# Kernel optimization log

Measured on AMD Instinct MI355X. Metric: run time of the kernel, lower is better.

The kernel has to match this reference:

```python
import jax, jax.numpy as jnp
import numpy as np

B, L, E, H = 2, 2048, 1024, 16
D = E // H  # head_dim = 64


def setup_inputs() -> dict:
    key = jax.random.key(0)
    ks = jax.random.split(key, 9)
    s = 1.0 / np.sqrt(E)
    return {
        "query": jax.random.normal(ks[0], (B, L, E), jnp.float32),
        "key": jax.random.normal(ks[1], (B, L, E), jnp.float32),
        "value": jax.random.normal(ks[2], (B, L, E), jnp.float32),
        # torch Linear weights are [out_features, in_features]
        "Wq": jax.random.uniform(ks[3], (E, E), jnp.float32, -s, s),
        "bq": jnp.zeros((E,), jnp.float32),
        "Wk": jax.random.uniform(ks[4], (E, E), jnp.float32, -s, s),  # k_proj, no bias (add_bias_kv=False)
        "Wv": jax.random.uniform(ks[5], (E, E), jnp.float32, -s, s),  # v_proj, no bias
        "Wo": jax.random.uniform(ks[6], (E, E), jnp.float32, -s, s),
        "bo": jnp.zeros((E,), jnp.float32),
    }


def reference(query, key, value, Wq, bq, Wk, Wv, Wo, bo):
    # Projections (torch Linear: y = x @ W.T + b)
    q = query @ Wq.T + bq          # [B, L, E]
    k = key @ Wk.T                 # [B, L, E]
    v = value @ Wv.T               # [B, L, E]
    # Split heads
    q = q.reshape(B, L, H, D)
    k = k.reshape(B, L, H, D)
    v = v.reshape(B, L, H, D)
    # Scaled dot-product attention; the source's chunked online-softmax
    # computes exactly softmax(q k^T / sqrt(D)) v.
    q = q / jnp.sqrt(jnp.asarray(D, q.dtype))
    scores = jnp.einsum("bqhd,bkhd->bhqk", q, k)      # [B, H, L, L]
    probs = jax.nn.softmax(scores, axis=-1)
    out = jnp.einsum("bhqk,bkhd->bqhd", probs, v)     # [B, L, H, D]
    out = out.reshape(B, L, E)
    return out @ Wo.T + bo
```

## Files before the change

kernel.cpp:

```cpp
#include <hip/hip_runtime.h>

typedef __bf16 bf16;
typedef __bf16 bf16x8 __attribute__((ext_vector_type(8)));
typedef __bf16 bf16x4 __attribute__((ext_vector_type(4)));
typedef float  f32x4  __attribute__((ext_vector_type(4)));

#define MFMA_BF16(a, b, c) __builtin_amdgcn_mfma_f32_16x16x32_bf16((a), (b), (c), 0, 0, 0)


__device__ __forceinline__ void async_load16(const bf16* g, const bf16* l) {
    auto gp = (const __attribute__((address_space(1))) unsigned int*)(unsigned long long)(const void*)g;
    auto lp = (__attribute__((address_space(3))) unsigned int*)(unsigned int)(unsigned long long)(const void*)l;
    __builtin_amdgcn_global_load_lds(gp, lp, 16, 0, 0);
}

__global__ void cvt_bf16_kernel(
    const float* __restrict__ s0, const float* __restrict__ s1, const float* __restrict__ s2,
    const float* __restrict__ s3, const float* __restrict__ s4, const float* __restrict__ s5,
    const float* __restrict__ s6,
    bf16* __restrict__ d0, bf16* __restrict__ d1, bf16* __restrict__ d2,
    bf16* __restrict__ d3, bf16* __restrict__ d4, bf16* __restrict__ d5,
    bf16* __restrict__ d6)
{
    const float* src; bf16* dst; int n;
    switch (blockIdx.y) {
        case 0: src = s0; dst = d0; n = 4194304; break;
        case 1: src = s1; dst = d1; n = 4194304; break;
        case 2: src = s2; dst = d2; n = 4194304; break;
        case 3: src = s3; dst = d3; n = 1048576; break;
        case 4: src = s4; dst = d4; n = 1048576; break;
        case 5: src = s5; dst = d5; n = 1048576; break;
        default: src = s6; dst = d6; n = 1048576; break;
    }
    int i = (blockIdx.x * 256 + threadIdx.x) * 4;
    if (i >= n) return;
    float4 f = *(const float4*)(src + i);
    bf16x4 o;
    o.x = (bf16)f.x; o.y = (bf16)f.y; o.z = (bf16)f.z; o.w = (bf16)f.w;
    *(bf16x4*)(dst + i) = o;
}

template<int BN>
__global__ __launch_bounds__(256, (BN == 128) ? 2 : 4) void gemm4_kernel(
    const bf16* __restrict__ Xq, const bf16* __restrict__ Xk, const bf16* __restrict__ Xv,
    const bf16* __restrict__ Ao,
    const bf16* __restrict__ Wq, const bf16* __restrict__ Wk, const bf16* __restrict__ Wv,
    const bf16* __restrict__ Wo,
    const float* __restrict__ bq, const float* __restrict__ bo,
    bf16* __restrict__ Qs, bf16* __restrict__ Ksw, bf16* __restrict__ Vsw,
    float* __restrict__ out, int zbase)
{
    const int z = zbase + blockIdx.z;
    const bf16 *Amat, *Bmat;
    if (z == 0)      { Amat = Wq; Bmat = Xq; }
    else if (z == 1) { Amat = Wk; Bmat = Xk; }
    else if (z == 2) { Amat = Xv; Bmat = Wv; }
    else             { Amat = Wo; Bmat = Ao; }

    const int m0 = (z == 2 ? blockIdx.y : blockIdx.x) * 128;
    const int n0 = (z == 2 ? blockIdx.x : blockIdx.y) * BN;

    __shared__ __align__(16) bf16 lA[128 * 32];
    __shared__ __align__(16) bf16 lB[BN * 32];

    const int tid  = threadIdx.x;
    const int w    = tid >> 6;
    const int lane = tid & 63;
    const int lm   = lane & 15;
    const int g    = lane >> 4;
    const int wm   = (w & 1) * 64;
    const int wn   = (w >> 1) * (BN / 2);
    constexpr int NT = BN / 32;
    constexpr int T  = (128 + BN) / 64;

    f32x4 acc[4][NT] = {};

    for (int kb = 0; kb < 32; kb++) {
        __syncthreads();
#pragma unroll
        for (int t = 0; t < T; t++) {
            int s   = (t * 4 + w) * 64 + lane;
            int row = s >> 2;
            int gs  = s & 3;
            int gg  = gs ^ ((row >> 1) & 3);
            if (row < 128)
                async_load16(Amat + (size_t)(m0 + row) * 1024 + kb * 32 + gg * 8, lA + s * 8);
            else
                async_load16(Bmat + (size_t)(n0 + row - 128) * 1024 + kb * 32 + gg * 8,
                             lB + (s - 512) * 8);
        }
        __syncthreads();

        bf16x8 af[4], bfr[NT];
#pragma unroll
        for (int mt = 0; mt < 4; mt++) {
            int row = wm + mt * 16 + lm;
            af[mt] = *(const bf16x8*)(lA + row * 32 + ((g ^ ((row >> 1) & 3)) << 3));
        }
#pragma unroll
        for (int nt = 0; nt < NT; nt++) {
            int row = wn + nt * 16 + lm;
            bfr[nt] = *(const bf16x8*)(lB + row * 32 + ((g ^ ((row >> 1) & 3)) << 3));
        }
#pragma unroll
        for (int mt = 0; mt < 4; mt++)
#pragma unroll
            for (int nt = 0; nt < NT; nt++)
                acc[mt][nt] = MFMA_BF16(af[mt], bfr[nt], acc[mt][nt]);
    }

    if (z == 3) {
#pragma unroll
        for (int mt = 0; mt < 4; mt++) {
            int mb = m0 + wm + mt * 16 + g * 4;
            f32x4 bov = *(const f32x4*)(bo + mb);
#pragma unroll
            for (int nt = 0; nt < NT; nt++) {
                int n = n0 + wn + nt * 16 + lm;
                f32x4 val;
#pragma unroll
                for (int r = 0; r < 4; r++) val[r] = acc[mt][nt][r] + bov[r];
                *(f32x4*)(out + (size_t)n * 1024 + mb) = val;
            }
        }
    } else if (z == 2) {
#pragma unroll
        for (int mt = 0; mt < 4; mt++) {
            int mb   = m0 + wm + mt * 16 + g * 4;
            int b    = mb >> 11;
            int lpos = mb & 2047;
            int kb2  = lpos >> 6, kc = (lpos >> 5) & 1, gv = (lpos >> 3) & 3, j0 = lpos & 7;
#pragma unroll
            for (int nt = 0; nt < NT; nt++) {
                int n = n0 + wn + nt * 16 + lm;
                int h = n >> 6, mt2 = (n >> 4) & 3, lmv = n & 15;
                bf16x4 ov;
#pragma unroll
                for (int r = 0; r < 4; r++) ov[r] = (bf16)acc[mt][nt][r];
                *(bf16x4*)(Vsw + (size_t)(b * 16 + h) * 131072 +
                           (size_t)((kb2 * 8 + mt2 * 2 + kc) * 64 + gv * 16 + lmv) * 8 + j0) = ov;
            }
        }
    } else if (z == 1) {
#pragma unroll
        for (int mt = 0; mt < 4; mt++) {
            int mb = m0 + wm + mt * 16 + g * 4;
            int h  = mb >> 6;
            int f  = (mb >> 5) & 1, gk = (mb >> 3) & 3, j0 = mb & 7;
#pragma unroll
            for (int nt = 0; nt < NT; nt++) {
                int n    = n0 + wn + nt * 16 + lm;
                int b    = n >> 11;
                int lpos = n & 2047;
                int kb2  = lpos >> 6;
                int rem  = lpos & 63;
                int c    = ((rem >> 4) & 2) | ((rem >> 2) & 1);
                int lmk  = ((rem >> 1) & 12) | (rem & 3);
                bf16x4 ov;
#pragma unroll
                for (int r = 0; r < 4; r++) ov[r] = (bf16)acc[mt][nt][r];
                *(bf16x4*)(Ksw + (size_t)(b * 16 + h) * 131072 +
                           (size_t)((kb2 * 8 + c * 2 + f) * 64 + gk * 16 + lmk) * 8 + j0) = ov;
            }
        }
    } else {
        const float qscale = 0.18033688011112042f;
#pragma unroll
        for (int mt = 0; mt < 4; mt++) {
            int mb  = m0 + wm + mt * 16 + g * 4;
            int h   = mb >> 6;
            int dd0 = mb & 63;
            f32x4 bqv = *(const f32x4*)(bq + mb);
#pragma unroll
            for (int nt = 0; nt < NT; nt++) {
                int n    = n0 + wn + nt * 16 + lm;
                int b    = n >> 11;
                int lpos = n & 2047;
                bf16x4 ov;
#pragma unroll
                for (int r = 0; r < 4; r++)
                    ov[r] = (bf16)((acc[mt][nt][r] + bqv[r]) * qscale);
                *(bf16x4*)(Qs + (size_t)((b * 16 + h) * 2048 + lpos) * 64 + dd0) = ov;
            }
        }
    }
}

__global__ __launch_bounds__(128, 4) void attn_kernel(
    const bf16* __restrict__ Qs, const bf16* __restrict__ Ksw,
    const bf16* __restrict__ Vsw, bf16* __restrict__ attn)
{
    const int w    = threadIdx.x >> 6;
    const int lane = threadIdx.x & 63;
    const int lm   = lane & 15;
    const int g    = lane >> 4;
    const int i    = blockIdx.x;
    const int bh   = ((i & 7) << 2) | ((i >> 3) & 3);
    const int q0   = (i >> 5) * 32;

    const bf16* Qh = Qs  + (size_t)bh * (2048 * 64);
    const bf16* kp = Ksw + (size_t)bh * (2048 * 64) + (size_t)(w * 16) * 4096 + (size_t)lane * 8;
    const bf16* vp = Vsw + (size_t)bh * (2048 * 64) + (size_t)(w * 16) * 4096 + (size_t)lane * 8;

    bf16x8 qf[2][2];
#pragma unroll
    for (int qi = 0; qi < 2; qi++)
#pragma unroll
        for (int f = 0; f < 2; f++)
            qf[qi][f] = *(const bf16x8*)(Qh + (size_t)(q0 + qi * 16 + lm) * 64 + f * 32 + g * 8);

    bf16x8 ones;
#pragma unroll
    for (int j = 0; j < 8; j++) ones[j] = (bf16)1.0f;
    const f32x4 fzero = {0.0f, 0.0f, 0.0f, 0.0f};

    f32x4 o[2][4] = {};
    f32x4 lacc[2] = {};

    bf16x8 kf[4][2];
#pragma unroll
    for (int c = 0; c < 4; c++)
#pragma unroll
        for (int f = 0; f < 2; f++)
            kf[c][f] = *(const bf16x8*)(kp + (c * 2 + f) * 512);

    for (int kb = 0; kb < 16; kb++) {
        f32x4 s[2][4];
#pragma unroll
        for (int c = 0; c < 4; c++) {
            s[0][c] = MFMA_BF16(kf[c][0], qf[0][0], fzero);
            s[1][c] = MFMA_BF16(kf[c][0], qf[1][0], fzero);
            s[0][c] = MFMA_BF16(kf[c][1], qf[0][1], s[0][c]);
            s[1][c] = MFMA_BF16(kf[c][1], qf[1][1], s[1][c]);
        }

        bf16x8 vf[4][2];
#pragma unroll
        for (int mt = 0; mt < 4; mt++)
#pragma unroll
            for (int kc = 0; kc < 2; kc++)
                vf[mt][kc] = *(const bf16x8*)(vp + (mt * 2 + kc) * 512);
        vp += 4096;

        kp += 4096;
        if (kb < 15) {
#pragma unroll
            for (int c = 0; c < 4; c++)
#pragma unroll
                for (int f = 0; f < 2; f++)
                    kf[c][f] = *(const bf16x8*)(kp + (c * 2 + f) * 512);
        }

        bf16x8 pb[2][2];
#pragma unroll
        for (int qi = 0; qi < 2; qi++)
#pragma unroll
            for (int kc = 0; kc < 2; kc++)
#pragma unroll
                for (int r = 0; r < 4; r++) {
                    pb[qi][kc][r]     = (bf16)__builtin_amdgcn_exp2f(s[qi][2 * kc][r]);
                    pb[qi][kc][r + 4] = (bf16)__builtin_amdgcn_exp2f(s[qi][2 * kc + 1][r]);
                }

#pragma unroll
        for (int kc = 0; kc < 2; kc++) {
            lacc[0] = MFMA_BF16(ones, pb[0][kc], lacc[0]);
            lacc[1] = MFMA_BF16(ones, pb[1][kc], lacc[1]);
#pragma unroll
            for (int mt = 0; mt < 4; mt++) {
                o[0][mt] = MFMA_BF16(vf[mt][kc], pb[0][kc], o[0][mt]);
                o[1][mt] = MFMA_BF16(vf[mt][kc], pb[1][kc], o[1][mt]);
            }
        }
    }

    __shared__ float part[64 * 36];
    __shared__ __align__(16) bf16 ost[32 * 72];
    if (w == 1) {
        float* p = part + lane * 36;
#pragma unroll
        for (int qi = 0; qi < 2; qi++)
#pragma unroll
            for (int mt = 0; mt < 4; mt++)
                *(f32x4*)(p + (qi * 4 + mt) * 4) = o[qi][mt];
        p[32] = lacc[0][0];
        p[33] = lacc[1][0];
    }
    __syncthreads();
    if (w == 0) {
        const float* p = part + lane * 36;
#pragma unroll
        for (int qi = 0; qi < 2; qi++)
#pragma unroll
            for (int mt = 0; mt < 4; mt++) {
                f32x4 t = *(const f32x4*)(p + (qi * 4 + mt) * 4);
#pragma unroll
                for (int r = 0; r < 4; r++) o[qi][mt][r] += t[r];
            }
        float inv0 = 1.0f / (lacc[0][0] + p[32]);
        float inv1 = 1.0f / (lacc[1][0] + p[33]);

#pragma unroll
        for (int qi = 0; qi < 2; qi++) {
            float inv = qi ? inv1 : inv0;
#pragma unroll
            for (int mt = 0; mt < 4; mt++) {
                bf16x4 ov;
#pragma unroll
                for (int r = 0; r < 4; r++) ov[r] = (bf16)(o[qi][mt][r] * inv);
                *(bf16x4*)(ost + (qi * 16 + lm) * 72 + mt * 16 + g * 4) = ov;
            }
        }
        const int b = bh >> 4, h = bh & 15;
#pragma unroll
        for (int it = 0; it < 4; it++) {
            int cc = it * 64 + lane;
            int q  = cc >> 3, ch = cc & 7;
            bf16x8 t = *(const bf16x8*)(ost + q * 72 + ch * 8);
            *(bf16x8*)(attn + (size_t)(b * 2048 + q0 + q) * 1024 + h * 64 + ch * 8) = t;
        }
    }
}

extern "C" void kernel_launch(void* const* d_in, const int* in_sizes, int n_in,
                              void* d_out, int out_size, void* d_ws, size_t ws_size,
                              hipStream_t stream) {
    const float* query = (const float*)d_in[0];
    const float* key   = (const float*)d_in[1];
    const float* value = (const float*)d_in[2];
    const float* Wq    = (const float*)d_in[3];
    const float* bq    = (const float*)d_in[4];
    const float* Wk    = (const float*)d_in[5];
    const float* Wv    = (const float*)d_in[6];
    const float* Wo    = (const float*)d_in[7];
    const float* bo    = (const float*)d_in[8];

    char* ws = (char*)d_ws;
    bf16* Xq  = (bf16*)(ws);
    bf16* Xk  = (bf16*)(ws + ((size_t)8  << 20));
    bf16* Xv  = (bf16*)(ws + ((size_t)16 << 20));
    bf16* Wqb = (bf16*)(ws + ((size_t)24 << 20));
    bf16* Wkb = (bf16*)(ws + ((size_t)26 << 20));
    bf16* Wvb = (bf16*)(ws + ((size_t)28 << 20));
    bf16* Wob = (bf16*)(ws + ((size_t)30 << 20));
    bf16* Qs  = (bf16*)(ws + ((size_t)32 << 20));
    bf16* Ksw = (bf16*)(ws + ((size_t)40 << 20));
    bf16* Vsw = (bf16*)(ws + ((size_t)48 << 20));
    bf16* attn = Xq;

    cvt_bf16_kernel<<<dim3(4096, 7, 1), 256, 0, stream>>>(
        query, key, value, Wq, Wk, Wv, Wo, Xq, Xk, Xv, Wqb, Wkb, Wvb, Wob);

    gemm4_kernel<128><<<dim3(8, 32, 3), 256, 0, stream>>>(
        Xq, Xk, Xv, attn, Wqb, Wkb, Wvb, Wob, bq, bo, Qs, Ksw, Vsw, (float*)d_out, 0);

    attn_kernel<<<dim3(2048, 1, 1), 128, 0, stream>>>(Qs, Ksw, Vsw, attn);

    gemm4_kernel<64><<<dim3(8, 64, 1), 256, 0, stream>>>(
        Xq, Xk, Xv, attn, Wqb, Wkb, Wvb, Wob, bq, bo, Qs, Ksw, Vsw, (float*)d_out, 3);
}
```

Before: 214.8 us.

## Flatten conversion grid, raise GEMM occupancy, sum softmax denominators with VALU

The fp32-to-bf16 conversion kernel now runs on a flat 1D grid sized exactly to the element count, so it no longer launches idle blocks for the smaller weight tensors. The BN=128 projection GEMM's launch bounds go from 2 to 3 blocks per SM, which may limit registers. In attention, the MFMA-with-ones that accumulated the softmax row sum is replaced by fp32 VALU adds of the exponentials and a cross-lane shuffle reduction, removing four MFMAs per key block. The denominator is now summed from fp32 values rather than the bf16-rounded ones, which slightly changes numerics.

```diff
diff --git a/kernel.cpp b/kernel.cpp
--- a/kernel.cpp
+++ b/kernel.cpp
@@ -22,26 +22,28 @@
     bf16* __restrict__ d3, bf16* __restrict__ d4, bf16* __restrict__ d5,
     bf16* __restrict__ d6)
 {
-    const float* src; bf16* dst; int n;
-    switch (blockIdx.y) {
-        case 0: src = s0; dst = d0; n = 4194304; break;
-        case 1: src = s1; dst = d1; n = 4194304; break;
-        case 2: src = s2; dst = d2; n = 4194304; break;
-        case 3: src = s3; dst = d3; n = 1048576; break;
-        case 4: src = s4; dst = d4; n = 1048576; break;
-        case 5: src = s5; dst = d5; n = 1048576; break;
-        default: src = s6; dst = d6; n = 1048576; break;
-    }
-    int i = (blockIdx.x * 256 + threadIdx.x) * 4;
-    if (i >= n) return;
-    float4 f = *(const float4*)(src + i);
+    unsigned e = (blockIdx.x * 256 + threadIdx.x) * 4;
+    const float* src; bf16* dst; unsigned off;
+    if (e < 12582912u) {
+        unsigned which = e >> 22;
+        src = which == 0 ? s0 : (which == 1 ? s1 : s2);
+        dst = which == 0 ? d0 : (which == 1 ? d1 : d2);
+        off = e & 4194303u;
+    } else {
+        unsigned ew = e - 12582912u;
+        unsigned which = ew >> 20;
+        src = which == 0 ? s3 : (which == 1 ? s4 : (which == 2 ? s5 : s6));
+        dst = which == 0 ? d3 : (which == 1 ? d4 : (which == 2 ? d5 : d6));
+        off = ew & 1048575u;
+    }
+    float4 f = *(const float4*)(src + off);
     bf16x4 o;
     o.x = (bf16)f.x; o.y = (bf16)f.y; o.z = (bf16)f.z; o.w = (bf16)f.w;
-    *(bf16x4*)(dst + i) = o;
+    *(bf16x4*)(dst + off) = o;
 }
 
 template<int BN>
-__global__ __launch_bounds__(256, (BN == 128) ? 2 : 4) void gemm4_kernel(
+__global__ __launch_bounds__(256, (BN == 128) ? 3 : 4) void gemm4_kernel(
     const bf16* __restrict__ Xq, const bf16* __restrict__ Xk, const bf16* __restrict__ Xv,
     const bf16* __restrict__ Ao,
     const bf16* __restrict__ Wq, const bf16* __restrict__ Wk, const bf16* __restrict__ Wv,
@@ -198,9 +200,9 @@
     const int bh   = ((i & 7) << 2) | ((i >> 3) & 3);
     const int q0   = (i >> 5) * 32;
 
-    const bf16* Qh = Qs  + (size_t)bh * (2048 * 64);
-    const bf16* kp = Ksw + (size_t)bh * (2048 * 64) + (size_t)(w * 16) * 4096 + (size_t)lane * 8;
-    const bf16* vp = Vsw + (size_t)bh * (2048 * 64) + (size_t)(w * 16) * 4096 + (size_t)lane * 8;
+    const bf16* Qh = Qs  + (size_t)bh * 131072;
+    const bf16* kp = Ksw + (size_t)bh * 131072 + (size_t)(w * 16) * 4096 + (size_t)lane * 8;
+    const bf16* vp = Vsw + (size_t)bh * 131072 + (size_t)(w * 16) * 4096 + (size_t)lane * 8;
 
     bf16x8 qf[2][2];
 #pragma unroll
@@ -209,13 +211,9 @@
         for (int f = 0; f < 2; f++)
             qf[qi][f] = *(const bf16x8*)(Qh + (size_t)(q0 + qi * 16 + lm) * 64 + f * 32 + g * 8);
 
-    bf16x8 ones;
-#pragma unroll
-    for (int j = 0; j < 8; j++) ones[j] = (bf16)1.0f;
     const f32x4 fzero = {0.0f, 0.0f, 0.0f, 0.0f};
-
     f32x4 o[2][4] = {};
-    f32x4 lacc[2] = {};
+    float lsum[2] = {0.0f, 0.0f};
 
     bf16x8 kf[4][2];
 #pragma unroll
@@ -253,25 +251,34 @@
 
         bf16x8 pb[2][2];
 #pragma unroll
-        for (int qi = 0; qi < 2; qi++)
+        for (int qi = 0; qi < 2; qi++) {
+            float part = 0.0f;
 #pragma unroll
             for (int kc = 0; kc < 2; kc++)
 #pragma unroll
                 for (int r = 0; r < 4; r++) {
-                    pb[qi][kc][r]     = (bf16)__builtin_amdgcn_exp2f(s[qi][2 * kc][r]);
-                    pb[qi][kc][r + 4] = (bf16)__builtin_amdgcn_exp2f(s[qi][2 * kc + 1][r]);
+                    float p0 = __builtin_amdgcn_exp2f(s[qi][2 * kc][r]);
+                    float p1 = __builtin_amdgcn_exp2f(s[qi][2 * kc + 1][r]);
+                    pb[qi][kc][r]     = (bf16)p0;
+                    pb[qi][kc][r + 4] = (bf16)p1;
+                    part += p0 + p1;
                 }
-
-#pragma unroll
-        for (int kc = 0; kc < 2; kc++) {
-            lacc[0] = MFMA_BF16(ones, pb[0][kc], lacc[0]);
-            lacc[1] = MFMA_BF16(ones, pb[1][kc], lacc[1]);
+            lsum[qi] += part;
+        }
+
+#pragma unroll
+        for (int kc = 0; kc < 2; kc++)
 #pragma unroll
             for (int mt = 0; mt < 4; mt++) {
                 o[0][mt] = MFMA_BF16(vf[mt][kc], pb[0][kc], o[0][mt]);
                 o[1][mt] = MFMA_BF16(vf[mt][kc], pb[1][kc], o[1][mt]);
             }
-        }
+    }
+
+#pragma unroll
+    for (int qi = 0; qi < 2; qi++) {
+        lsum[qi] += __shfl_xor(lsum[qi], 16);
+        lsum[qi] += __shfl_xor(lsum[qi], 32);
     }
 
     __shared__ float part[64 * 36];
@@ -283,8 +290,8 @@
 #pragma unroll
             for (int mt = 0; mt < 4; mt++)
                 *(f32x4*)(p + (qi * 4 + mt) * 4) = o[qi][mt];
-        p[32] = lacc[0][0];
-        p[33] = lacc[1][0];
+        p[32] = lsum[0];
+        p[33] = lsum[1];
     }
     __syncthreads();
     if (w == 0) {
@@ -297,8 +304,8 @@
 #pragma unroll
                 for (int r = 0; r < 4; r++) o[qi][mt][r] += t[r];
             }
-        float inv0 = 1.0f / (lacc[0][0] + p[32]);
-        float inv1 = 1.0f / (lacc[1][0] + p[33]);
+        float inv0 = 1.0f / (lsum[0] + p[32]);
+        float inv1 = 1.0f / (lsum[1] + p[33]);
 
 #pragma unroll
         for (int qi = 0; qi < 2; qi++) {
@@ -348,7 +355,7 @@
     bf16* Vsw = (bf16*)(ws + ((size_t)48 << 20));
     bf16* attn = Xq;
 
-    cvt_bf16_kernel<<<dim3(4096, 7, 1), 256, 0, stream>>>(
+    cvt_bf16_kernel<<<dim3(16384, 1, 1), 256, 0, stream>>>(
         query, key, value, Wq, Wk, Wv, Wo, Xq, Xk, Xv, Wqb, Wkb, Wvb, Wob);
 
     gemm4_kernel<128><<<dim3(8, 32, 3), 256, 0, stream>>>(
```

Measured after the change: 216.9 us. About the same (+1.0%).
